# Kernel tuning notes

Measured on AMD Instinct MI355X. Metric: run time of the kernel, lower is better.

Reference implementation:

```python
import jax, jax.numpy as jnp
import numpy as np

N = 20000      # atom nodes
N_LG = 40000   # line-graph nodes (= undirected bonds)
E = 80000      # directed edges in original graph (= 2*N_LG)
E_LG = 200000  # line-graph edges
L = 5          # num_layer
D = 300        # emb_dim
NUM_ATOM, NUM_BOND, NUM_DIR, NUM_CHI = 120, 6, 3, 3
EPS = 1e-5


def setup_inputs() -> dict:
    key = jax.random.key(0)
    ks = jax.random.split(key, 24)
    ri = lambda k, shape, hi: jax.random.randint(k, shape, 0, hi, dtype=jnp.int32)
    nm = lambda k, shape: jax.random.normal(k, shape, dtype=jnp.float32) * 0.02
    inp = {}
    inp["x"] = ri(ks[0], (N, 2), 3)
    inp["edge_index"] = ri(ks[1], (2, E), N)
    inp["edge_attr"] = ri(ks[2], (E, 2), 3)
    inp["lg_x"] = ri(ks[3], (N_LG, 2), 3)
    inp["lg_edge_index"] = ri(ks[4], (2, E_LG), N_LG)
    inp["lg_edge_index_map"] = ri(ks[5], (2, N_LG), N)
    inp["lg_edge_index_map2"] = ri(ks[6], (E_LG,), N)
    # GNN-level embeddings
    inp["node_emb1"] = nm(ks[7], (NUM_ATOM, D))
    inp["node_emb2"] = nm(ks[8], (NUM_CHI, D))
    inp["gnn_edge_emb1"] = nm(ks[9], (NUM_BOND, D))
    inp["gnn_edge_emb2"] = nm(ks[10], (NUM_DIR, D))
    # per-layer main-graph GINConv params (stacked over layers)
    inp["g_emb1"] = nm(ks[11], (L, NUM_BOND, D))
    inp["g_emb2"] = nm(ks[12], (L, NUM_DIR, D))
    inp["g_w1"] = nm(ks[13], (L, D, 2 * D))
    inp["g_b1"] = jnp.zeros((L, 2 * D), jnp.float32)
    inp["g_w2"] = nm(ks[14], (L, 2 * D, D))
    inp["g_b2"] = jnp.zeros((L, D), jnp.float32)
    inp["g_gamma"] = jnp.ones((L, D), jnp.float32)
    inp["g_beta"] = jnp.zeros((L, D), jnp.float32)
    # per-layer line-graph GINConv params (is_lg=True -> atom/chirality tables)
    inp["lg_emb1"] = nm(ks[15], (L, NUM_ATOM, D))
    inp["lg_emb2"] = nm(ks[16], (L, NUM_CHI, D))
    inp["lg_w1"] = nm(ks[17], (L, D, 2 * D))
    inp["lg_b1"] = jnp.zeros((L, 2 * D), jnp.float32)
    inp["lg_w2"] = nm(ks[18], (L, 2 * D, D))
    inp["lg_b2"] = jnp.zeros((L, D), jnp.float32)
    inp["lg_gamma"] = jnp.ones((L, D), jnp.float32)
    inp["lg_beta"] = jnp.zeros((L, D), jnp.float32)
    return inp


def gin_conv(xn, src, dst, ea, emb1, emb2, sl_idx, w1, b1, w2, b2):
    # self loops appended at the end, with self_loop_attr = emb1[sl_idx] + emb2[0]
    n = xn.shape[0]
    sl = jnp.broadcast_to(emb1[sl_idx] + emb2[0], (n, xn.shape[1]))
    ea_full = jnp.concatenate([ea, sl], axis=0)
    idx = jnp.arange(n, dtype=src.dtype)
    src_f = jnp.concatenate([src, idx])
    dst_f = jnp.concatenate([dst, idx])
    msg = xn[src_f] + ea_full                      # gather + add
    aggr = jax.ops.segment_sum(msg, dst_f, num_segments=n)  # scatter-add
    return jnp.maximum(aggr @ w1 + b1, 0.0) @ w2 + b2        # MLP update


def batchnorm(h, g, b):
    # training-mode BN: batch mean / biased variance (matches torch normalization)
    mu = h.mean(0)
    var = h.var(0)
    return (h - mu) * jax.lax.rsqrt(var + EPS) * g + b


def reference(x, edge_index, edge_attr, lg_x, lg_edge_index, lg_edge_index_map,
              lg_edge_index_map2, node_emb1, node_emb2, gnn_edge_emb1, gnn_edge_emb2,
              g_emb1, g_emb2, g_w1, g_b1, g_w2, g_b2, g_gamma, g_beta,
              lg_emb1, lg_emb2, lg_w1, lg_b1, lg_w2, lg_b2, lg_gamma, lg_beta):
    h = node_emb1[x[:, 0]] + node_emb2[x[:, 1]]
    e = gnn_edge_emb1[lg_x[:, 0]] + gnn_edge_emb2[lg_x[:, 1]]
    h_list, e_list = [h], [e]
    lg_src, lg_dst = lg_edge_index[0], lg_edge_index[1]
    for layer in range(L):
        if layer == 0:
            ea = g_emb1[0][edge_attr[:, 0]] + g_emb2[0][edge_attr[:, 1]]
            src, dst = edge_index[0], edge_index[1]
        else:
            # edge_index rewritten from line-graph map; edge_attr = cat([e, e])
            ea = jnp.concatenate([e_list[layer], e_list[layer]], axis=0)
            src = jnp.concatenate([lg_edge_index_map[0], lg_edge_index_map[1]])
            dst = jnp.concatenate([lg_edge_index_map[1], lg_edge_index_map[0]])
        h = gin_conv(h_list[layer], src, dst, ea, g_emb1[layer], g_emb2[layer], 4,
                     g_w1[layer], g_b1[layer], g_w2[layer], g_b2[layer])
        h = batchnorm(h, g_gamma[layer], g_beta[layer])
        if layer < L - 1:
            h = jnp.maximum(h, 0.0)
        h_list.append(h)
        if layer == 0:
            xa = x[lg_edge_index_map2]  # int atom features of shared node
            lg_ea = lg_emb1[0][xa[:, 0]] + lg_emb2[0][xa[:, 1]]
        else:
            # lg_edge_attr = h[lg_edge_index_map2] from the PREVIOUS iteration's h
            lg_ea = h_list[layer][lg_edge_index_map2]
        e = gin_conv(e_list[layer], lg_src, lg_dst, lg_ea, lg_emb1[layer], lg_emb2[layer], 119,
                     lg_w1[layer], lg_b1[layer], lg_w2[layer], lg_b2[layer])
        e = batchnorm(e, lg_gamma[layer], lg_beta[layer])
        if layer < L - 1:
            e = jnp.maximum(e, 0.0)
        e_list.append(e)
    # (h_list, e_list) packed as one array: [L+1, N + N_LG, D]
    return jnp.concatenate([jnp.stack(h_list), jnp.stack(e_list)], axis=1)
```

## Files before the change

### kernel.cpp

```cpp
#include <hip/hip_runtime.h>

#define D 300

namespace {

constexpr int kN   = 20000;
constexpr int kNLG = 40000;
constexpr int kE   = 80000;
constexpr int kELG = 200000;
constexpr int kL   = 5;

constexpr int K1P = 320;
constexpr int N1P = 640;
constexpr int K2P = 640;
constexpr int N2P = 384;
constexpr int MP_N   = 20096;
constexpr int MP_ALL = 60160;
constexpr int MAIN_TILES = 157;
constexpr int RH = 320;
constexpr int RQ = 40;

typedef __attribute__((ext_vector_type(8))) _Float16 half8;
typedef __attribute__((ext_vector_type(2))) _Float16 half2v;
typedef __attribute__((ext_vector_type(4))) float f32x4;

__device__ inline short f2h(float f) {
  _Float16 h = (_Float16)f;
  return __builtin_bit_cast(short, h);
}

__device__ inline float h2f(short s) {
  return (float)__builtin_bit_cast(_Float16, s);
}

__device__ inline float2 upk(unsigned u) {
  half2v h = __builtin_bit_cast(half2v, u);
  return make_float2((float)h.x, (float)h.y);
}

__device__ inline unsigned pk(float a, float b) {
  half2v h;
  h.x = (_Float16)a;
  h.y = (_Float16)b;
  return __builtin_bit_cast(unsigned, h);
}

__device__ inline void addrow(float* acc, uint4 r) {
  float2 t0 = upk(r.x), t1 = upk(r.y), t2 = upk(r.z), t3 = upk(r.w);
  acc[0] += t0.x; acc[1] += t0.y; acc[2] += t1.x; acc[3] += t1.y;
  acc[4] += t2.x; acc[5] += t2.y; acc[6] += t3.x; acc[7] += t3.y;
}

__device__ inline uint4 pk4(const float* a) {
  uint4 r;
  r.x = pk(a[0], a[1]); r.y = pk(a[2], a[3]);
  r.z = pk(a[4], a[5]); r.w = pk(a[6], a[7]);
  return r;
}

__device__ inline void gload_lds16(const void* g, void* l) {
  __builtin_amdgcn_global_load_lds(
      (const __attribute__((address_space(1))) void*)g,
      (__attribute__((address_space(3))) void*)l, 16, 0, 0);
}


__global__ void k_init(float* __restrict__ stats, short* __restrict__ ab,
                       int* __restrict__ m0_cur, int* __restrict__ mL_cur,
                       int* __restrict__ lg_cur) {
  int g = blockIdx.x * blockDim.x + threadIdx.x;
  if (g < kL * 1200) stats[g] = 0.f;
  int np1 = (MP_N - kN) * K1P;
  int np2 = (MP_ALL - MP_N - kNLG) * K1P;
  if (g < np1) ab[(size_t)kN * K1P + g] = 0;
  if (g < np2) ab[(size_t)(MP_N + kNLG) * K1P + g] = 0;
  if (g < kN) { m0_cur[g] = 0; mL_cur[g] = 0; }
  if (g < kNLG) lg_cur[g] = 0;
}


__global__ void k_hist_all(const int* __restrict__ edge_index,
                           const int* __restrict__ lg_map,
                           const int* __restrict__ lg_ei,
// ... 112 lines not shown

__device__ void cvt_w1(const float* W, short* Wt, int g) {
  int per = N1P * K1P;
  int l = g / per, rem = g - l * per;
  int n = rem / K1P, k = rem - n * K1P;
  float v = (n < 2 * D && k < D) ? W[(size_t)l * D * 2 * D + (size_t)k * 2 * D + n] : 0.f;
  Wt[g] = f2h(v);
}

__device__ void cvt_w2(const float* W, short* Wt, int g) {
  int per = N2P * K2P;
  int l = g / per, rem = g - l * per;
  int n = rem / K2P, k = rem - n * K2P;
  float v = (n < D && k < 2 * D) ? W[(size_t)l * 2 * D * D + (size_t)k * D + n] : 0.f;
  Wt[g] = f2h(v);
}

__global__ void k_convert_wt_all(const float* __restrict__ g_w1, const float* __restrict__ g_w2,
                                 const float* __restrict__ lg_w1, const float* __restrict__ lg_w2,
                                 short* __restrict__ g_w1t, short* __restrict__ g_w2t,
                                 short* __restrict__ lg_w1t, short* __restrict__ lg_w2t) {
  int g = blockIdx.x * blockDim.x + threadIdx.x;
  const int s1 = kL * N1P * K1P, s2 = kL * N2P * K2P;
  if (g < s1) { cvt_w1(g_w1, g_w1t, g); return; }
  g -= s1;
  if (g < s2) { cvt_w2(g_w2, g_w2t, g); return; }
  g -= s2;
  if (g < s1) { cvt_w1(lg_w1, lg_w1t, g); return; }
  g -= s1;
  if (g < s2) cvt_w2(lg_w2, lg_w2t, g);
}


__global__ void k_gather_all0(
    const uint4* __restrict__ h16, const uint4* __restrict__ e16,
    const int* __restrict__ m_src, const int* __restrict__ eattr,
    const int* __restrict__ x, const int* __restrict__ lg_src,
    const int* __restrict__ map2,
    const uint4* __restrict__ t1m, const uint4* __restrict__ t2m,
    const uint4* __restrict__ t1l, const uint4* __restrict__ t2l,
    const float* __restrict__ slvM, const float* __restrict__ slvL,
    const int* __restrict__ m_offs, const int* __restrict__ m_perm,
    const int* __restrict__ l_offs, const int* __restrict__ l_perm,
    uint4* __restrict__ ab) {
  int node = blockIdx.x * 4 + (threadIdx.x >> 6);
  int lane = threadIdx.x & 63;
  if (node >= kN + kNLG) return;
  bool act = lane < RQ;
  int ll = act ? lane : 0;
  bool isM = node < kN;
  int j = isM ? node : node - kN;
  const uint4* selfrow = isM ? (h16 + (size_t)node * RQ) : (e16 + (size_t)j * RQ);
  const float* sv = (isM ? slvM : slvL) + ll * 8;
  const int* offs = isM ? m_offs : l_offs;
  const int* permp = isM ? m_perm : l_perm;
  const uint4* bA = isM ? h16 : e16;
  const uint4* bT1 = isM ? t1m : t1l;
  const uint4* bT2 = isM ? t2m : t2l;

  float acc[8];
  {
    uint4 s = selfrow[ll];
    float2 t0 = upk(s.x), t1 = upk(s.y), t2 = upk(s.z), t3 = upk(s.w);
    acc[0] = t0.x + sv[0]; acc[1] = t0.y + sv[1];
    acc[2] = t1.x + sv[2]; acc[3] = t1.y + sv[3];
    acc[4] = t2.x + sv[4]; acc[5] = t2.y + sv[5];
    acc[6] = t3.x + sv[6]; acc[7] = t3.y + sv[7];
  }

  int p0 = offs[j], p1 = offs[j + 1];
  for (int pb = p0; pb < p1; pb += 64) {
    int cnt = min(64, p1 - pb);
    int e_ = permp[pb + ((lane < cnt) ? lane : 0)];
    int r1, r2, r3;
    if (isM) {
      r1 = m_src[e_];
      r2 = eattr[2 * e_];
      r3 = eattr[2 * e_ + 1];
    } else {
      r1 = lg_src[e_];
      int a = map2[e_];
      r2 = x[2 * a];
      r3 = x[2 * a + 1];
    }
    int t = 0;
    for (; t + 1 < cnt; t += 2) {
      int a0 = __shfl(r1, t), b0 = __shfl(r2, t), c0 = __shfl(r3, t);
      int a1 = __shfl(r1, t + 1), b1 = __shfl(r2, t + 1), c1 = __shfl(r3, t + 1);
      uint4 x0 = bA[(size_t)a0 * RQ + ll];
      uint4 y0 = bT1[(size_t)b0 * RQ + ll];
      uint4 z0 = bT2[(size_t)c0 * RQ + ll];
      uint4 x1 = bA[(size_t)a1 * RQ + ll];
      uint4 y1 = bT1[(size_t)b1 * RQ + ll];
      uint4 z1 = bT2[(size_t)c1 * RQ + ll];
      addrow(acc, x0); addrow(acc, y0); addrow(acc, z0);
      addrow(acc, x1); addrow(acc, y1); addrow(acc, z1);
    }
    if (t < cnt) {
      int a0 = __shfl(r1, t), b0 = __shfl(r2, t), c0 = __shfl(r3, t);
      uint4 x0 = bA[(size_t)a0 * RQ + ll];
      uint4 y0 = bT1[(size_t)b0 * RQ + ll];
      uint4 z0 = bT2[(size_t)c0 * RQ + ll];
      addrow(acc, x0); addrow(acc, y0); addrow(acc, z0);
    }
  }
  if (act) ab[(size_t)(isM ? node : MP_N + j) * RQ + ll] = pk4(acc);
}

__global__ void k_gather_allL(
    const uint4* __restrict__ h16, const uint4* __restrict__ e16,
    const int* __restrict__ lg_map, const int* __restrict__ lg_src,
    const int* __restrict__ map2,
    const float* __restrict__ slvM, const float* __restrict__ slvL,
    const int* __restrict__ m_offs, const int* __restrict__ m_perm,
    const int* __restrict__ l_offs, const int* __restrict__ l_perm,
    uint4* __restrict__ ab) {
  int node = blockIdx.x * 4 + (threadIdx.x >> 6);
  int lane = threadIdx.x & 63;
  if (node >= kN + kNLG) return;
  bool act = lane < RQ;
  int ll = act ? lane : 0;
  bool isM = node < kN;
  int j = isM ? node : node - kN;
  const uint4* selfrow = isM ? (h16 + (size_t)node * RQ) : (e16 + (size_t)j * RQ);
  const float* sv = (isM ? slvM : slvL) + ll * 8;
  const int* offs = isM ? m_offs : l_offs;
  const int* permp = isM ? m_perm : l_perm;
  const uint4* bA = isM ? h16 : e16;
  const uint4* bB = isM ? e16 : h16;

  float acc[8];
  {
    uint4 s = selfrow[ll];
    float2 t0 = upk(s.x), t1 = upk(s.y), t2 = upk(s.z), t3 = upk(s.w);
    acc[0] = t0.x + sv[0]; acc[1] = t0.y + sv[1];
    acc[2] = t1.x + sv[2]; acc[3] = t1.y + sv[3];
    acc[4] = t2.x + sv[4]; acc[5] = t2.y + sv[5];
    acc[6] = t3.x + sv[6]; acc[7] = t3.y + sv[7];
  }

  int p0 = offs[j], p1 = offs[j + 1];
  for (int pb = p0; pb < p1; pb += 64) {
    int cnt = min(64, p1 - pb);
    int e_ = permp[pb + ((lane < cnt) ? lane : 0)];
    int ra, rb;
    if (isM) {
      ra = lg_map[e_];
      rb = (e_ < kNLG) ? e_ : e_ - kNLG;
    } else {
      ra = lg_src[e_];
      rb = map2[e_];
    }
    int t = 0;
    for (; t + 3 < cnt; t += 4) {
      int a0 = __shfl(ra, t),     b0 = __shfl(rb, t);
      int a1 = __shfl(ra, t + 1), b1 = __shfl(rb, t + 1);
      int a2 = __shfl(ra, t + 2), b2 = __shfl(rb, t + 2);
      int a3 = __shfl(ra, t + 3), b3 = __shfl(rb, t + 3);
      uint4 x0 = bA[(size_t)a0 * RQ + ll];
      uint4 y0 = bB[(size_t)b0 * RQ + ll];
      uint4 x1 = bA[(size_t)a1 * RQ + ll];
      uint4 y1 = bB[(size_t)b1 * RQ + ll];
      uint4 x2 = bA[(size_t)a2 * RQ + ll];
      uint4 y2 = bB[(size_t)b2 * RQ + ll];
      uint4 x3 = bA[(size_t)a3 * RQ + ll];
      uint4 y3 = bB[(size_t)b3 * RQ + ll];
      addrow(acc, x0); addrow(acc, y0);
      addrow(acc, x1); addrow(acc, y1);
      addrow(acc, x2); addrow(acc, y2);
      addrow(acc, x3); addrow(acc, y3);
    }
    for (; t < cnt; ++t) {
      int a0 = __shfl(ra, t), b0 = __shfl(rb, t);
      uint4 x0 = bA[(size_t)a0 * RQ + ll];
      uint4 y0 = bB[(size_t)b0 * RQ + ll];
      addrow(acc, x0); addrow(acc, y0);
    }
  }
  if (act) ab[(size_t)(isM ? node : MP_N + j) * RQ + ll] = pk4(acc);
}


__global__ void k_embed_pair(const int* __restrict__ idx, const float* __restrict__ t1,
                             const float* __restrict__ t2, float* __restrict__ out,
                             short* __restrict__ hist, int n) {
  int g = blockIdx.x * blockDim.x + threadIdx.x;
  if (g >= n * RH) return;
  int i = g / RH, c = g - i * RH;
  short hv = 0;
  if (c < D) {
    float v = t1[(size_t)idx[2 * i] * D + c] + t2[(size_t)idx[2 * i + 1] * D + c];
    out[(size_t)i * D + c] = v;
    hv = f2h(v);
  }
  hist[g] = hv;
}


template<bool RELU, bool STATS>
__global__ __launch_bounds__(256) void k_mfma_gemm_dual(
    const short* __restrict__ A,
    const short* __restrict__ BtM, const short* __restrict__ BtL,
    const float* __restrict__ biasM, const float* __restrict__ biasL, int biasN,
    short* __restrict__ Cout, int Ccols, int Cstride, int Kpad,
    int mainLimit, int lgLimit,
    float* __restrict__ statsM, float* __restrict__ statsL) {
  __shared__ __align__(16) short ldsA[128 * 32];
  __shared__ __align__(16) short ldsB[128 * 32];
  __shared__ float sd[256];
  const int tid = threadIdx.x;
  const int lane = tid & 63, w = tid >> 6;
  const bool isMain = (int)blockIdx.y < MAIN_TILES;
  const short* Bt = isMain ? BtM : BtL;
  const float* bias = isMain ? biasM : biasL;
  const int rowLimit = isMain ? mainLimit : lgLimit;
  const int brow = blockIdx.y * 128;
  const int bcol = blockIdx.x * 128;
  const int wr = w >> 1, wc = w & 1;

  if (STATS) sd[tid] = 0.f;

  f32x4 acc[4][4] = {};

  const int sr = tid >> 2;
  const int sc = (tid & 3) * 8;
  char* la = (char*)ldsA + w * 1024;
  char* lb = (char*)ldsB + w * 1024;

  for (int k0 = 0; k0 < Kpad; k0 += 32) {
    __syncthreads();
    const short* gA0 = A + (size_t)(brow + sr) * Kpad + (k0 + sc);
    const short* gB0 = Bt + (size_t)(bcol + sr) * Kpad + (k0 + sc);
    gload_lds16(gA0, la);
    gload_lds16(gA0 + (size_t)64 * Kpad, la + 4096);
    gload_lds16(gB0, lb);
    gload_lds16(gB0 + (size_t)64 * Kpad, lb + 4096);
    __syncthreads();
// ... 2 lines not shown
    half8 af[4], bf[4];
#pragma unroll
    for (int m = 0; m < 4; ++m) {
      int row = wr * 64 + m * 16 + (lane & 15);
      af[m] = *(const half8*)((const char*)ldsA + row * 64 + kq);
    }
#pragma unroll
    for (int n = 0; n < 4; ++n) {
      int col = wc * 64 + n * 16 + (lane & 15);
      bf[n] = *(const half8*)((const char*)ldsB + col * 64 + kq);
    }
#pragma unroll
    for (int m = 0; m < 4; ++m)
#pragma unroll
      for (int n = 0; n < 4; ++n)
        acc[m][n] = __builtin_amdgcn_mfma_f32_16x16x32_f16(af[m], bf[n], acc[m][n], 0, 0, 0);
  }

  const int r0 = brow + wr * 64;
  const int c0 = bcol + wc * 64;
  float ps[4] = {}, pq[4] = {};
#pragma unroll
  for (int m = 0; m < 4; ++m) {
#pragma unroll
    for (int i = 0; i < 4; ++i) {
      int row = r0 + m * 16 + (lane >> 4) * 4 + i;
      bool rv = row < rowLimit;
#pragma unroll
      for (int n = 0; n < 4; ++n) {
        int col = c0 + n * 16 + (lane & 15);
        float bv = (col < biasN) ? bias[col] : 0.f;
        float v = acc[m][n][i] + bv;
        if (RELU) v = fmaxf(v, 0.f);
        if (rv && col < Ccols) {
          Cout[(size_t)row * Cstride + col] = f2h(v);
          if (STATS) { ps[n] += v; pq[n] += v * v; }
        }
      }
    }
  }

  if (STATS) {
#pragma unroll
    for (int n = 0; n < 4; ++n) {
      float s = ps[n], q = pq[n];
      s += __shfl_xor(s, 16); q += __shfl_xor(q, 16);
      s += __shfl_xor(s, 32); q += __shfl_xor(q, 32);
      if ((lane >> 4) == 0) {
        int c = wc * 64 + n * 16 + (lane & 15);
        atomicAdd(&sd[c], s);
        atomicAdd(&sd[128 + c], q);
      }
    }
    __syncthreads();
    float* gs = isMain ? statsM : statsL;
    if (tid < 128) {
      int col = bcol + tid;
      if (col < Ccols) {
        atomicAdd(&gs[col], sd[tid]);
        atomicAdd(&gs[D + col], sd[128 + tid]);
      }
    }
  }
}


template<bool WRITE_HIST>
__global__ void k_bn_apply_all(const short* __restrict__ pre, float* __restrict__ Xout,
                               short* __restrict__ hist,
                               const float* __restrict__ statsM,
                               const float* __restrict__ statsL,
                               const float* __restrict__ gM, const float* __restrict__ bM,
                               const float* __restrict__ gL, const float* __restrict__ bL,
                               int relu) {
  int g = blockIdx.x * blockDim.x + threadIdx.x;
  if (g >= (kN + kNLG) * RH) return;
  int r = g / RH;
  int c = g - r * RH;
  short hv = 0;
  if (c < D) {
    bool m = r < kN;
    int pr = m ? r : MP_N + (r - kN);
    const float* s = m ? statsM : statsL;
    float inv_n = m ? (1.f / kN) : (1.f / kNLG);
    float mu = s[c] * inv_n;
    float var = s[D + c] * inv_n - mu * mu;
    float rs = rsqrtf(var + 1e-5f);
    float gam = (m ? gM : gL)[c];
    float bet = (m ? bM : bL)[c];
    float v = (h2f(pre[(size_t)pr * N2P + c]) - mu) * rs * gam + bet;
    if (relu) v = fmaxf(v, 0.f);
    Xout[(size_t)r * D + c] = v;
    hv = f2h(v);
  }
  if (WRITE_HIST) hist[g] = hv;
}

}

extern "C" void kernel_launch(void* const* d_in, const int* in_sizes, int n_in,
                              void* d_out_v, int out_size, void* d_ws, size_t ws_size,
                              hipStream_t stream) {
  const int*   x            = (const int*)d_in[0];
  const int*   edge_index   = (const int*)d_in[1];
  const int*   edge_attr    = (const int*)d_in[2];
  const int*   lg_x         = (const int*)d_in[3];
  const int*   lg_edge_index= (const int*)d_in[4];
  const int*   lg_map       = (const int*)d_in[5];
  const int*   lg_map2      = (const int*)d_in[6];
  const float* node_emb1    = (const float*)d_in[7];
  const float* node_emb2    = (const float*)d_in[8];
  const float* gnn_e_emb1   = (const float*)d_in[9];
  const float* gnn_e_emb2   = (const float*)d_in[10];
  const float* g_emb1       = (const float*)d_in[11];
  const float* g_emb2       = (const float*)d_in[12];
  const float* g_w1         = (const float*)d_in[13];
  const float* g_b1         = (const float*)d_in[14];
  const float* g_w2         = (const float*)d_in[15];
  const float* g_b2         = (const float*)d_in[16];
  const float* g_gamma      = (const float*)d_in[17];
  const float* g_beta       = (const float*)d_in[18];
  const float* lg_emb1      = (const float*)d_in[19];
  const float* lg_emb2      = (const float*)d_in[20];
  const float* lg_w1        = (const float*)d_in[21];
  const float* lg_b1        = (const float*)d_in[22];
  const float* lg_w2        = (const float*)d_in[23];
  const float* lg_b2        = (const float*)d_in[24];
  const float* lg_gamma     = (const float*)d_in[25];
  const float* lg_beta      = (const float*)d_in[26];

  float* out = (float*)d_out_v;
  char*  ws  = (char*)d_ws;

  size_t off = 0;
  auto alloc = [&](size_t bytes) { void* p = ws + off; off = (off + bytes + 255) & ~(size_t)255; return p; };
  short* ab      = (short*)alloc((size_t)MP_ALL * K1P * 2);
  short* hidden  = (short*)alloc((size_t)MP_ALL * N1P * 2);
  short* pre16   = (short*)alloc((size_t)MP_ALL * N2P * 2);
  short* hist16  = (short*)alloc((size_t)(kL + 1) * 60000 * RH * 2);
  short* g_w1t   = (short*)alloc((size_t)kL * N1P * K1P * 2);
  short* g_w2t   = (short*)alloc((size_t)kL * N2P * K2P * 2);
  short* lg_w1t  = (short*)alloc((size_t)kL * N1P * K1P * 2);
  short* lg_w2t  = (short*)alloc((size_t)kL * N2P * K2P * 2);
  float* stats   = (float*)alloc(kL * 1200 * 4);
  float* slv     = (float*)alloc(kL * 640 * 4);
  short* t1m     = (short*)alloc(6 * RH * 2);
  short* t2m     = (short*)alloc(3 * RH * 2);
  short* t1l     = (short*)alloc(120 * RH * 2);
  short* t2l     = (short*)alloc(3 * RH * 2);
  int* m0_offs = (int*)alloc((kN + 1) * 4);
  int* m0_cur  = (int*)alloc(kN * 4);
  int* m0_perm = (int*)alloc(kE * 4);
  int* mL_offs = (int*)alloc((kN + 1) * 4);
  int* mL_cur  = (int*)alloc(kN * 4);
  int* mL_perm = (int*)alloc(2 * kNLG * 4);
  int* lg_offs = (int*)alloc((kNLG + 1) * 4);
  int* lg_cur  = (int*)alloc(kNLG * 4);
  int* lg_perm = (int*)alloc(kELG * 4);

  auto hptr  = [&](int l) { return out + (size_t)l * 60000 * D; };
  auto h16p  = [&](int l) { return hist16 + (size_t)l * 60000 * RH; };
  auto e16p  = [&](int l) { return hist16 + ((size_t)l * 60000 + kN) * RH; };

  dim3 b(256);

  k_init<<<(kNLG + 255) / 256, b, 0, stream>>>(stats, ab, m0_cur, mL_cur, lg_cur);
  {
    int tot = kE + 2 * kNLG + kELG;
    k_hist_all<<<(tot + 255) / 256, b, 0, stream>>>(edge_index, lg_map, lg_edge_index,
                                                    m0_cur, mL_cur, lg_cur);
    k_scan3<<<3, b, 0, stream>>>(m0_cur, m0_offs, mL_cur, mL_offs, lg_cur, lg_offs);
    k_fill_all<<<(tot + 255) / 256, b, 0, stream>>>(edge_index, lg_map, lg_edge_index,
                                                    m0_cur, m0_perm, mL_cur, mL_perm,
                                                    lg_cur, lg_perm);
  }
  k_selfvec<<<(kL * 640 + 255) / 256, b, 0, stream>>>(g_emb1, g_emb2, lg_emb1, lg_emb2, slv);
  k_pad_tab_all<<<(132 * RH + 255) / 256, b, 0, stream>>>(g_emb1, g_emb2, lg_emb1, lg_emb2,
                                                          t1m, t2m, t1l, t2l);
  {
    int tot = 2 * kL * (N1P * K1P + N2P * K2P);
    k_convert_wt_all<<<(tot + 255) / 256, b, 0, stream>>>(g_w1, g_w2, lg_w1, lg_w2,
                                                          g_w1t, g_w2t, lg_w1t, lg_w2t);
  }
  k_embed_pair<<<(kN * RH + 255) / 256, b, 0, stream>>>(x, node_emb1, node_emb2,
                                                        hptr(0), h16p(0), kN);
  k_embed_pair<<<(kNLG * RH + 255) / 256, b, 0, stream>>>(lg_x, gnn_e_emb1, gnn_e_emb2,
                                                          hptr(0) + (size_t)kN * D,
                                                          e16p(0), kNLG);

  for (int l = 0; l < kL; ++l) {
    int relu_tail = (l < kL - 1) ? 1 : 0;
    float* slot = stats + (size_t)l * 1200;
    const float* slvM = slv + (size_t)l * 640;
    const float* slvL = slvM + 320;

    if (l == 0)
      k_gather_all0<<<(kN + kNLG + 3) / 4, b, 0, stream>>>(
          (const uint4*)h16p(0), (const uint4*)e16p(0),
          edge_index, edge_attr, x, lg_edge_index, lg_map2,
          (const uint4*)t1m, (const uint4*)t2m, (const uint4*)t1l, (const uint4*)t2l,
          slvM, slvL, m0_offs, m0_perm, lg_offs, lg_perm, (uint4*)ab);
    else
      k_gather_allL<<<(kN + kNLG + 3) / 4, b, 0, stream>>>(
          (const uint4*)h16p(l), (const uint4*)e16p(l),
          lg_map, lg_edge_index, lg_map2,
          slvM, slvL, mL_offs, mL_perm, lg_offs, lg_perm, (uint4*)ab);

    k_mfma_gemm_dual<true, false><<<dim3(N1P / 128, MP_ALL / 128), b, 0, stream>>>(
        ab, g_w1t + (size_t)l * N1P * K1P, lg_w1t + (size_t)l * N1P * K1P,
        g_b1 + (size_t)l * 2 * D, lg_b1 + (size_t)l * 2 * D, 2 * D,
        hidden, N1P, N1P, K1P, MP_ALL, MP_ALL, nullptr, nullptr);

    k_mfma_gemm_dual<false, true><<<dim3(N2P / 128, MP_ALL / 128), b, 0, stream>>>(
        hidden, g_w2t + (size_t)l * N2P * K2P, lg_w2t + (size_t)l * N2P * K2P,
        g_b2 + (size_t)l * D, lg_b2 + (size_t)l * D, D,
        pre16, D, N2P, K2P, kN, MP_N + kNLG,
        slot, slot + 600);

    if (l < kL - 1)
      k_bn_apply_all<true><<<((kN + kNLG) * RH + 255) / 256, b, 0, stream>>>(
          pre16, hptr(l + 1), h16p(l + 1), slot, slot + 600,
          g_gamma + (size_t)l * D, g_beta + (size_t)l * D,
          lg_gamma + (size_t)l * D, lg_beta + (size_t)l * D, relu_tail);
    else
      k_bn_apply_all<false><<<((kN + kNLG) * RH + 255) / 256, b, 0, stream>>>(
          pre16, hptr(l + 1), h16p(l + 1), slot, slot + 600,
          g_gamma + (size_t)l * D, g_beta + (size_t)l * D,
          lg_gamma + (size_t)l * D, lg_beta + (size_t)l * D, relu_tail);
  }
}
```

Measured before the change: 1.539 ms.

## Fuse batchnorm apply into next layer's gather, drop fp16 history buffers

Removes the per-layer batchnorm-apply kernel. The next layer's gather now reads the raw fp16 GEMM output, recomputes the BN scale and shift from the stats, and applies BN plus ReLU to every gathered neighbour row. The self-row pass writes the fp32 output for the previous layer, and a separate final kernel handles the last layer without ReLU. The second GEMM now writes a narrower 320-column pre-activation buffer instead of 384. This saves a full read/write pass and the fp16 history storage per layer. In exchange, the gather does extra FMA and max work per neighbour and the unroll drops from 4 to 2.

```diff
diff --git a/kernel.cpp b/kernel.cpp
--- a/kernel.cpp
+++ b/kernel.cpp
@@ -14,6 +14,7 @@
 constexpr int N1P = 640;
 constexpr int K2P = 640;
 constexpr int N2P = 384;
+constexpr int PQH = 320;
 constexpr int MP_N   = 20096;
 constexpr int MP_ALL = 60160;
 constexpr int MAIN_TILES = 157;
@@ -49,6 +50,12 @@
   float2 t0 = upk(r.x), t1 = upk(r.y), t2 = upk(r.z), t3 = upk(r.w);
   acc[0] += t0.x; acc[1] += t0.y; acc[2] += t1.x; acc[3] += t1.y;
   acc[4] += t2.x; acc[5] += t2.y; acc[6] += t3.x; acc[7] += t3.y;
+}
+
+__device__ inline void unpk8(uint4 r, float* v) {
+  float2 t0 = upk(r.x), t1 = upk(r.y), t2 = upk(r.z), t3 = upk(r.w);
+  v[0] = t0.x; v[1] = t0.y; v[2] = t1.x; v[3] = t1.y;
+  v[4] = t2.x; v[5] = t2.y; v[6] = t3.x; v[7] = t3.y;
 }
 
 __device__ inline uint4 pk4(const float* a) {
@@ -255,12 +262,10 @@
 
   float acc[8];
   {
-    uint4 s = selfrow[ll];
-    float2 t0 = upk(s.x), t1 = upk(s.y), t2 = upk(s.z), t3 = upk(s.w);
-    acc[0] = t0.x + sv[0]; acc[1] = t0.y + sv[1];
-    acc[2] = t1.x + sv[2]; acc[3] = t1.y + sv[3];
-    acc[4] = t2.x + sv[4]; acc[5] = t2.y + sv[5];
-    acc[6] = t3.x + sv[6]; acc[7] = t3.y + sv[7];
+    float vv[8];
+    unpk8(selfrow[ll], vv);
+#pragma unroll
+    for (int i = 0; i < 8; ++i) acc[i] = vv[i] + sv[i];
   }
 
   int p0 = offs[j], p1 = offs[j + 1];
@@ -302,14 +307,18 @@
   if (act) ab[(size_t)(isM ? node : MP_N + j) * RQ + ll] = pk4(acc);
 }
 
-__global__ void k_gather_allL(
-    const uint4* __restrict__ h16, const uint4* __restrict__ e16,
+
+__global__ void k_gather_bn(
+    const uint4* __restrict__ pre,
     const int* __restrict__ lg_map, const int* __restrict__ lg_src,
     const int* __restrict__ map2,
+    const float* __restrict__ sM, const float* __restrict__ sL,
+    const float* __restrict__ gaM, const float* __restrict__ beM,
+    const float* __restrict__ gaL, const float* __restrict__ beL,
     const float* __restrict__ slvM, const float* __restrict__ slvL,
     const int* __restrict__ m_offs, const int* __restrict__ m_perm,
     const int* __restrict__ l_offs, const int* __restrict__ l_perm,
-    uint4* __restrict__ ab) {
+    float* __restrict__ outF, uint4* __restrict__ ab) {
   int node = blockIdx.x * 4 + (threadIdx.x >> 6);
   int lane = threadIdx.x & 63;
   if (node >= kN + kNLG) return;
@@ -317,59 +326,97 @@
   int ll = act ? lane : 0;
   bool isM = node < kN;
   int j = isM ? node : node - kN;
-  const uint4* selfrow = isM ? (h16 + (size_t)node * RQ) : (e16 + (size_t)j * RQ);
+
+  float aM[8], bM[8], aL[8], bL[8];
+#pragma unroll
+  for (int i = 0; i < 8; ++i) {
+    int c = ll * 8 + i;
+    if (c < D) {
+      float muM = sM[c] * (1.f / kN);
+      float vaM = sM[D + c] * (1.f / kN) - muM * muM;
+      float am = rsqrtf(vaM + 1e-5f) * gaM[c];
+      aM[i] = am; bM[i] = beM[c] - muM * am;
+      float muL = sL[c] * (1.f / kNLG);
+      float vaL = sL[D + c] * (1.f / kNLG) - muL * muL;
+      float al = rsqrtf(vaL + 1e-5f) * gaL[c];
+      aL[i] = al; bL[i] = beL[c] - muL * al;
+    } else {
+      aM[i] = bM[i] = aL[i] = bL[i] = 0.f;
+    }
+  }
+
   const float* sv = (isM ? slvM : slvL) + ll * 8;
   const int* offs = isM ? m_offs : l_offs;
   const int* permp = isM ? m_perm : l_perm;
-  const uint4* bA = isM ? h16 : e16;
-  const uint4* bB = isM ? e16 : h16;
 
   float acc[8];
   {
-    uint4 s = selfrow[ll];
-    float2 t0 = upk(s.x), t1 = upk(s.y), t2 = upk(s.z), t3 = upk(s.w);
-    acc[0] = t0.x + sv[0]; acc[1] = t0.y + sv[1];
-    acc[2] = t1.x + sv[2]; acc[3] = t1.y + sv[3];
-    acc[4] = t2.x + sv[4]; acc[5] = t2.y + sv[5];
-    acc[6] = t3.x + sv[6]; acc[7] = t3.y + sv[7];
+    int selfRow = isM ? node : MP_N + j;
+    float vv[8], y[8];
+    unpk8(pre[(size_t)selfRow * RQ + ll], vv);
+#pragma unroll
+    for (int i = 0; i < 8; ++i) {
+      float a = isM ? aM[i] : aL[i];
+      float b = isM ? bM[i] : bL[i];
+      y[i] = fmaxf(a * vv[i] + b, 0.f);
+      acc[i] = y[i] + sv[i];
+    }
+    if (act) {
+      float* op = outF + (size_t)node * D + ll * 8;
+      if (ll < 37) {
+        *(float4*)op = make_float4(y[0], y[1], y[2], y[3]);
+        *(float4*)(op + 4) = make_float4(y[4], y[5], y[6], y[7]);
+      } else if (ll == 37) {
+        *(float4*)op = make_float4(y[0], y[1], y[2], y[3]);
+      }
+    }
   }
 
   int p0 = offs[j], p1 = offs[j + 1];
   for (int pb = p0; pb < p1; pb += 64) {
     int cnt = min(64, p1 - pb);
     int e_ = permp[pb + ((lane < cnt) ? lane : 0)];
-    int ra, rb;
+    int rh, re;
     if (isM) {
-      ra = lg_map[e_];
-      rb = (e_ < kNLG) ? e_ : e_ - kNLG;
+      rh = lg_map[e_];
+      re = MP_N + ((e_ < kNLG) ? e_ : e_ - kNLG);
     } else {
-      ra = lg_src[e_];
-      rb = map2[e_];
+      rh = map2[e_];
+      re = MP_N + lg_src[e_];
     }
     int t = 0;
-    for (; t + 3 < cnt; t += 4) {
-      int a0 = __shfl(ra, t),     b0 = __shfl(rb, t);
-      int a1 = __shfl(ra, t + 1), b1 = __shfl(rb, t + 1);
-      int a2 = __shfl(ra, t + 2), b2 = __shfl(rb, t + 2);
-      int a3 = __shfl(ra, t + 3), b3 = __shfl(rb, t + 3);
-      uint4 x0 = bA[(size_t)a0 * RQ + ll];
-      uint4 y0 = bB[(size_t)b0 * RQ + ll];
-      uint4 x1 = bA[(size_t)a1 * RQ + ll];
-      uint4 y1 = bB[(size_t)b1 * RQ + ll];
-      uint4 x2 = bA[(size_t)a2 * RQ + ll];
-      uint4 y2 = bB[(size_t)b2 * RQ + ll];
-      uint4 x3 = bA[(size_t)a3 * RQ + ll];
-      uint4 y3 = bB[(size_t)b3 * RQ + ll];
-      addrow(acc, x0); addrow(acc, y0);
-      addrow(acc, x1); addrow(acc, y1);
-      addrow(acc, x2); addrow(acc, y2);
-      addrow(acc, x3); addrow(acc, y3);
-    }
-    for (; t < cnt; ++t) {
-      int a0 = __shfl(ra, t), b0 = __shfl(rb, t);
-      uint4 x0 = bA[(size_t)a0 * RQ + ll];
-      uint4 y0 = bB[(size_t)b0 * RQ + ll];
-      addrow(acc, x0); addrow(acc, y0);
+    for (; t + 1 < cnt; t += 2) {
+      int h0 = __shfl(rh, t),     e0 = __shfl(re, t);
+      int h1 = __shfl(rh, t + 1), e1 = __shfl(re, t + 1);
+      uint4 xh0 = pre[(size_t)h0 * RQ + ll];
+      uint4 xe0 = pre[(size_t)e0 * RQ + ll];
+      uint4 xh1 = pre[(size_t)h1 * RQ + ll];
+      uint4 xe1 = pre[(size_t)e1 * RQ + ll];
+      float v[8];
+      unpk8(xh0, v);
+#pragma unroll
+      for (int i = 0; i < 8; ++i) acc[i] += fmaxf(aM[i] * v[i] + bM[i], 0.f);
+      unpk8(xe0, v);
+#pragma unroll
+      for (int i = 0; i < 8; ++i) acc[i] += fmaxf(aL[i] * v[i] + bL[i], 0.f);
+      unpk8(xh1, v);
+#pragma unroll
+      for (int i = 0; i < 8; ++i) acc[i] += fmaxf(aM[i] * v[i] + bM[i], 0.f);
+      unpk8(xe1, v);
+#pragma unroll
+      for (int i = 0; i < 8; ++i) acc[i] += fmaxf(aL[i] * v[i] + bL[i], 0.f);
+    }
+    if (t < cnt) {
+      int h0 = __shfl(rh, t), e0 = __shfl(re, t);
+      uint4 xh0 = pre[(size_t)h0 * RQ + ll];
+      uint4 xe0 = pre[(size_t)e0 * RQ + ll];
+      float v[8];
+      unpk8(xh0, v);
+#pragma unroll
+      for (int i = 0; i < 8; ++i) acc[i] += fmaxf(aM[i] * v[i] + bM[i], 0.f);
+      unpk8(xe0, v);
+#pragma unroll
+      for (int i = 0; i < 8; ++i) acc[i] += fmaxf(aL[i] * v[i] + bL[i], 0.f);
     }
   }
   if (act) ab[(size_t)(isM ? node : MP_N + j) * RQ + ll] = pk4(acc);
@@ -397,7 +444,7 @@
     const short* __restrict__ A,
     const short* __restrict__ BtM, const short* __restrict__ BtL,
     const float* __restrict__ biasM, const float* __restrict__ biasL, int biasN,
-    short* __restrict__ Cout, int Ccols, int Cstride, int Kpad,
+    short* __restrict__ Cout, int Cstat, int Cwrite, int Cstride, int Kpad,
     int mainLimit, int lgLimit,
     float* __restrict__ statsM, float* __restrict__ statsL) {
   __shared__ __align__(16) short ldsA[128 * 32];
@@ -466,9 +513,9 @@
         float bv = (col < biasN) ? bias[col] : 0.f;
         float v = acc[m][n][i] + bv;
         if (RELU) v = fmaxf(v, 0.f);
-        if (rv && col < Ccols) {
+        if (rv && col < Cwrite) {
           Cout[(size_t)row * Cstride + col] = f2h(v);
-          if (STATS) { ps[n] += v; pq[n] += v * v; }
+          if (STATS && col < Cstat) { ps[n] += v; pq[n] += v * v; }
         }
       }
     }
@@ -490,7 +537,7 @@
     float* gs = isMain ? statsM : statsL;
     if (tid < 128) {
       int col = bcol + tid;
-      if (col < Ccols) {
+      if (col < Cstat) {
         atomicAdd(&gs[col], sd[tid]);
         atomicAdd(&gs[D + col], sd[128 + tid]);
       }
@@ -499,35 +546,24 @@
 }
 
 
-template<bool WRITE_HIST>
-__global__ void k_bn_apply_all(const short* __restrict__ pre, float* __restrict__ Xout,
-                               short* __restrict__ hist,
-                               const float* __restrict__ statsM,
-                               const float* __restrict__ statsL,
-                               const float* __restrict__ gM, const float* __restrict__ bM,
-                               const float* __restrict__ gL, const float* __restrict__ bL,
-                               int relu) {
+__global__ void k_bn_final(const short* __restrict__ pre, float* __restrict__ Xout,
+                           const float* __restrict__ sM, const float* __restrict__ sL,
+                           const float* __restrict__ gM, const float* __restrict__ bM,
+                           const float* __restrict__ gL, const float* __restrict__ bL) {
   int g = blockIdx.x * blockDim.x + threadIdx.x;
-  if (g >= (kN + kNLG) * RH) return;
-  int r = g / RH;
-  int c = g - r * RH;
-  short hv = 0;
-  if (c < D) {
-    bool m = r < kN;
-    int pr = m ? r : MP_N + (r - kN);
-    const float* s = m ? statsM : statsL;
-    float inv_n = m ? (1.f / kN) : (1.f / kNLG);
-    float mu = s[c] * inv_n;
-    float var = s[D + c] * inv_n - mu * mu;
-    float rs = rsqrtf(var + 1e-5f);
-    float gam = (m ? gM : gL)[c];
-    float bet = (m ? bM : bL)[c];
-    float v = (h2f(pre[(size_t)pr * N2P + c]) - mu) * rs * gam + bet;
-    if (relu) v = fmaxf(v, 0.f);
-    Xout[(size_t)r * D + c] = v;
-    hv = f2h(v);
-  }
-  if (WRITE_HIST) hist[g] = hv;
+  if (g >= (kN + kNLG) * D) return;
+  int r = g / D;
+  int c = g - r * D;
+  bool m = r < kN;
+  int pr = m ? r : MP_N + (r - kN);
+  const float* s = m ? sM : sL;
+  float inv_n = m ? (1.f / kN) : (1.f / kNLG);
+  float mu = s[c] * inv_n;
+  float var = s[D + c] * inv_n - mu * mu;
+  float rs = rsqrtf(var + 1e-5f);
+  float gam = (m ? gM : gL)[c];
+  float bet = (m ? bM : bL)[c];
+  Xout[g] = (h2f(pre[(size_t)pr * PQH + c]) - mu) * rs * gam + bet;
 }
 
 }
@@ -570,8 +606,8 @@
   auto alloc = [&](size_t bytes) { void* p = ws + off; off = (off + bytes + 255) & ~(size_t)255; return p; };
   short* ab      = (short*)alloc((size_t)MP_ALL * K1P * 2);
   short* hidden  = (short*)alloc((size_t)MP_ALL * N1P * 2);
-  short* pre16   = (short*)alloc((size_t)MP_ALL * N2P * 2);
-  short* hist16  = (short*)alloc((size_t)(kL + 1) * 60000 * RH * 2);
+  short* pre16   = (short*)alloc((size_t)MP_ALL * PQH * 2);
+  short* init16  = (short*)alloc((size_t)60000 * RH * 2);
   short* g_w1t   = (short*)alloc((size_t)kL * N1P * K1P * 2);
   short* g_w2t   = (short*)alloc((size_t)kL * N2P * K2P * 2);
   short* lg_w1t  = (short*)alloc((size_t)kL * N1P * K1P * 2);
@@ -592,9 +628,7 @@
   int* lg_cur  = (int*)alloc(kNLG * 4);
   int* lg_perm = (int*)alloc(kELG * 4);
 
-  auto hptr  = [&](int l) { return out + (size_t)l * 60000 * D; };
-  auto h16p  = [&](int l) { return hist16 + (size_t)l * 60000 * RH; };
-  auto e16p  = [&](int l) { return hist16 + ((size_t)l * 60000 + kN) * RH; };
+  auto hptr = [&](int l) { return out + (size_t)l * 60000 * D; };
 
   dim3 b(256);
 
@@ -617,49 +651,50 @@
                                                           g_w1t, g_w2t, lg_w1t, lg_w2t);
   }
   k_embed_pair<<<(kN * RH + 255) / 256, b, 0, stream>>>(x, node_emb1, node_emb2,
-                                                        hptr(0), h16p(0), kN);
+                                                        hptr(0), init16, kN);
   k_embed_pair<<<(kNLG * RH + 255) / 256, b, 0, stream>>>(lg_x, gnn_e_emb1, gnn_e_emb2,
                                                           hptr(0) + (size_t)kN * D,
-                                                          e16p(0), kNLG);
+                                                          init16 + (size_t)kN * RH, kNLG);
 
   for (int l = 0; l < kL; ++l) {
-    int relu_tail = (l < kL - 1) ? 1 : 0;
     float* slot = stats + (size_t)l * 1200;
     const float* slvM = slv + (size_t)l * 640;
     const float* slvL = slvM + 320;
 
-    if (l == 0)
+    if (l == 0) {
       k_gather_all0<<<(kN + kNLG + 3) / 4, b, 0, stream>>>(
-          (const uint4*)h16p(0), (const uint4*)e16p(0),
+          (const uint4*)init16, (const uint4*)(init16 + (size_t)kN * RH),
           edge_index, edge_attr, x, lg_edge_index, lg_map2,
           (const uint4*)t1m, (const uint4*)t2m, (const uint4*)t1l, (const uint4*)t2l,
           slvM, slvL, m0_offs, m0_perm, lg_offs, lg_perm, (uint4*)ab);
-    else
-      k_gather_allL<<<(kN + kNLG + 3) / 4, b, 0, stream>>>(
-          (const uint4*)h16p(l), (const uint4*)e16p(l),
-          lg_map, lg_edge_index, lg_map2,
-          slvM, slvL, mL_offs, mL_perm, lg_offs, lg_perm, (uint4*)ab);
+    } else {
+      float* pslot = stats + (size_t)(l - 1) * 1200;
+      k_gather_bn<<<(kN + kNLG + 3) / 4, b, 0, stream>>>(
+          (const uint4*)pre16, lg_map, lg_edge_index, lg_map2,
+          pslot, pslot + 600,
+          g_gamma + (size_t)(l - 1) * D, g_beta + (size_t)(l - 1) * D,
+          lg_gamma + (size_t)(l - 1) * D, lg_beta + (size_t)(l - 1) * D,
+          slvM, slvL, mL_offs, mL_perm, lg_offs, lg_perm,
+          hptr(l), (uint4*)ab);
+    }
 
     k_mfma_gemm_dual<true, false><<<dim3(N1P / 128, MP_ALL / 128), b, 0, stream>>>(
         ab, g_w1t + (size_t)l * N1P * K1P, lg_w1t + (size_t)l * N1P * K1P,
         g_b1 + (size_t)l * 2 * D, lg_b1 + (size_t)l * 2 * D, 2 * D,
-        hidden, N1P, N1P, K1P, MP_ALL, MP_ALL, nullptr, nullptr);
+        hidden, 0, N1P, N1P, K1P, MP_ALL, MP_ALL, nullptr, nullptr);
 
     k_mfma_gemm_dual<false, true><<<dim3(N2P / 128, MP_ALL / 128), b, 0, stream>>>(
         hidden, g_w2t + (size_t)l * N2P * K2P, lg_w2t + (size_t)l * N2P * K2P,
         g_b2 + (size_t)l * D, lg_b2 + (size_t)l * D, D,
-        pre16, D, N2P, K2P, kN, MP_N + kNLG,
+        pre16, D, PQH, PQH, K2P, kN, MP_N + kNLG,
         slot, slot + 600);
-
-    if (l < kL - 1)
-      k_bn_apply_all<true><<<((kN + kNLG) * RH + 255) / 256, b, 0, stream>>>(
-          pre16, hptr(l + 1), h16p(l + 1), slot, slot + 600,
-          g_gamma + (size_t)l * D, g_beta + (size_t)l * D,
-          lg_gamma + (size_t)l * D, lg_beta + (size_t)l * D, relu_tail);
-    else
-      k_bn_apply_all<false><<<((kN + kNLG) * RH + 255) / 256, b, 0, stream>>>(
-          pre16, hptr(l + 1), h16p(l + 1), slot, slot + 600,
-          g_gamma + (size_t)l * D, g_beta + (size_t)l * D,
-          lg_gamma + (size_t)l * D, lg_beta + (size_t)l * D, relu_tail);
-  }
-}
+  }
+
+  {
+    float* slot = stats + (size_t)(kL - 1) * 1200;
+    k_bn_final<<<((kN + kNLG) * D + 255) / 256, b, 0, stream>>>(
+        pre16, hptr(kL), slot, slot + 600,
+        g_gamma + (size_t)(kL - 1) * D, g_beta + (size_t)(kL - 1) * D,
+        lg_gamma + (size_t)(kL - 1) * D, lg_beta + (size_t)(kL - 1) * D);
+  }
+}
```

Result: slower. 2.276 ms (+47.9%).

## Vectorize batchnorm apply and embedding, precompute BN coefficients, double-buffer fp16 history

Applied to the files above, without the earlier changes.

Replaces the per-element batchnorm apply kernel with a vectorized one that handles 8 halves per thread, using per-column scale and shift computed once by a new small k_bn_coef kernel. The pre-activation buffer stride shrinks from 384 to 320 halves. The two embedding launches are merged into one vectorized kernel, and the fp16 history moves from a per-layer array to two ping-pong slots. The aim is fewer, wider memory transactions, no repeated mean/var/rsqrt per element, and a smaller workspace, at the cost of one extra tiny launch per layer.

```diff
diff --git a/kernel.cpp b/kernel.cpp
--- a/kernel.cpp
+++ b/kernel.cpp
@@ -14,11 +14,13 @@
 constexpr int N1P = 640;
 constexpr int K2P = 640;
 constexpr int N2P = 384;
+constexpr int PQH = 320;
 constexpr int MP_N   = 20096;
 constexpr int MP_ALL = 60160;
 constexpr int MAIN_TILES = 157;
 constexpr int RH = 320;
 constexpr int RQ = 40;
+constexpr int NALL = kN + kNLG;
 
 typedef __attribute__((ext_vector_type(8))) _Float16 half8;
 typedef __attribute__((ext_vector_type(2))) _Float16 half2v;
@@ -27,10 +29,6 @@
 __device__ inline short f2h(float f) {
   _Float16 h = (_Float16)f;
   return __builtin_bit_cast(short, h);
-}
-
-__device__ inline float h2f(short s) {
-  return (float)__builtin_bit_cast(_Float16, s);
 }
 
 __device__ inline float2 upk(unsigned u) {
@@ -49,6 +47,12 @@
   float2 t0 = upk(r.x), t1 = upk(r.y), t2 = upk(r.z), t3 = upk(r.w);
   acc[0] += t0.x; acc[1] += t0.y; acc[2] += t1.x; acc[3] += t1.y;
   acc[4] += t2.x; acc[5] += t2.y; acc[6] += t3.x; acc[7] += t3.y;
+}
+
+__device__ inline void unpk8(uint4 r, float* v) {
+  float2 t0 = upk(r.x), t1 = upk(r.y), t2 = upk(r.z), t3 = upk(r.w);
+  v[0] = t0.x; v[1] = t0.y; v[2] = t1.x; v[3] = t1.y;
+  v[4] = t2.x; v[5] = t2.y; v[6] = t3.x; v[7] = t3.y;
 }
 
 __device__ inline uint4 pk4(const float* a) {
@@ -227,6 +231,36 @@
 }
 
 
+__global__ void k_embed_all(const int* __restrict__ x, const int* __restrict__ lg_x,
+                            const float* __restrict__ t1m, const float* __restrict__ t2m,
+                            const float* __restrict__ t1l, const float* __restrict__ t2l,
+                            float* __restrict__ outF, uint4* __restrict__ hist) {
+  int g = blockIdx.x * blockDim.x + threadIdx.x;
+  if (g >= NALL * RQ) return;
+  int r = g / RQ, q = g - r * RQ;
+  bool m = r < kN;
+  int i = m ? r : r - kN;
+  const int* ix = (m ? x : lg_x) + 2 * i;
+  const float* t1 = (m ? t1m : t1l) + (size_t)ix[0] * D;
+  const float* t2 = (m ? t2m : t2l) + (size_t)ix[1] * D;
+  int c0 = q * 8;
+  float y[8] = {0.f, 0.f, 0.f, 0.f, 0.f, 0.f, 0.f, 0.f};
+  if (c0 < D) {
+    float4 p0 = *(const float4*)(t1 + c0);
+    float4 q0 = *(const float4*)(t2 + c0);
+    y[0] = p0.x + q0.x; y[1] = p0.y + q0.y; y[2] = p0.z + q0.z; y[3] = p0.w + q0.w;
+    *(float4*)(outF + (size_t)r * D + c0) = make_float4(y[0], y[1], y[2], y[3]);
+    if (c0 + 8 <= D) {
+      float4 p1 = *(const float4*)(t1 + c0 + 4);
+      float4 q1 = *(const float4*)(t2 + c0 + 4);
+      y[4] = p1.x + q1.x; y[5] = p1.y + q1.y; y[6] = p1.z + q1.z; y[7] = p1.w + q1.w;
+      *(float4*)(outF + (size_t)r * D + c0 + 4) = make_float4(y[4], y[5], y[6], y[7]);
+    }
+  }
+  hist[(size_t)r * RQ + q] = pk4(y);
+}
+
+
 __global__ void k_gather_all0(
     const uint4* __restrict__ h16, const uint4* __restrict__ e16,
     const int* __restrict__ m_src, const int* __restrict__ eattr,
@@ -240,7 +274,7 @@
     uint4* __restrict__ ab) {
   int node = blockIdx.x * 4 + (threadIdx.x >> 6);
   int lane = threadIdx.x & 63;
-  if (node >= kN + kNLG) return;
+  if (node >= NALL) return;
   bool act = lane < RQ;
   int ll = act ? lane : 0;
   bool isM = node < kN;
@@ -255,12 +289,10 @@
 
   float acc[8];
   {
-    uint4 s = selfrow[ll];
-    float2 t0 = upk(s.x), t1 = upk(s.y), t2 = upk(s.z), t3 = upk(s.w);
-    acc[0] = t0.x + sv[0]; acc[1] = t0.y + sv[1];
-    acc[2] = t1.x + sv[2]; acc[3] = t1.y + sv[3];
-    acc[4] = t2.x + sv[4]; acc[5] = t2.y + sv[5];
-    acc[6] = t3.x + sv[6]; acc[7] = t3.y + sv[7];
+    float vv[8];
+    unpk8(selfrow[ll], vv);
+#pragma unroll
+    for (int i = 0; i < 8; ++i) acc[i] = vv[i] + sv[i];
   }
 
   int p0 = offs[j], p1 = offs[j + 1];
@@ -302,6 +334,7 @@
   if (act) ab[(size_t)(isM ? node : MP_N + j) * RQ + ll] = pk4(acc);
 }
 
+
 __global__ void k_gather_allL(
     const uint4* __restrict__ h16, const uint4* __restrict__ e16,
     const int* __restrict__ lg_map, const int* __restrict__ lg_src,
@@ -312,7 +345,7 @@
     uint4* __restrict__ ab) {
   int node = blockIdx.x * 4 + (threadIdx.x >> 6);
   int lane = threadIdx.x & 63;
-  if (node >= kN + kNLG) return;
+  if (node >= NALL) return;
   bool act = lane < RQ;
   int ll = act ? lane : 0;
   bool isM = node < kN;
@@ -326,12 +359,10 @@
 
   float acc[8];
   {
-    uint4 s = selfrow[ll];
-    float2 t0 = upk(s.x), t1 = upk(s.y), t2 = upk(s.z), t3 = upk(s.w);
-    acc[0] = t0.x + sv[0]; acc[1] = t0.y + sv[1];
-    acc[2] = t1.x + sv[2]; acc[3] = t1.y + sv[3];
-    acc[4] = t2.x + sv[4]; acc[5] = t2.y + sv[5];
-    acc[6] = t3.x + sv[6]; acc[7] = t3.y + sv[7];
+    float vv[8];
+    unpk8(selfrow[ll], vv);
+#pragma unroll
+    for (int i = 0; i < 8; ++i) acc[i] = vv[i] + sv[i];
   }
 
   int p0 = offs[j], p1 = offs[j + 1];
@@ -376,28 +407,12 @@
 }
 
 
-__global__ void k_embed_pair(const int* __restrict__ idx, const float* __restrict__ t1,
-                             const float* __restrict__ t2, float* __restrict__ out,
-                             short* __restrict__ hist, int n) {
-  int g = blockIdx.x * blockDim.x + threadIdx.x;
-  if (g >= n * RH) return;
-  int i = g / RH, c = g - i * RH;
-  short hv = 0;
-  if (c < D) {
-    float v = t1[(size_t)idx[2 * i] * D + c] + t2[(size_t)idx[2 * i + 1] * D + c];
-    out[(size_t)i * D + c] = v;
-    hv = f2h(v);
-  }
-  hist[g] = hv;
-}
-
-
 template<bool RELU, bool STATS>
 __global__ __launch_bounds__(256) void k_mfma_gemm_dual(
     const short* __restrict__ A,
     const short* __restrict__ BtM, const short* __restrict__ BtL,
     const float* __restrict__ biasM, const float* __restrict__ biasL, int biasN,
-    short* __restrict__ Cout, int Ccols, int Cstride, int Kpad,
+    short* __restrict__ Cout, int Cstat, int Cwrite, int Cstride, int Kpad,
     int mainLimit, int lgLimit,
     float* __restrict__ statsM, float* __restrict__ statsL) {
   __shared__ __align__(16) short ldsA[128 * 32];
@@ -466,9 +481,9 @@
         float bv = (col < biasN) ? bias[col] : 0.f;
         float v = acc[m][n][i] + bv;
         if (RELU) v = fmaxf(v, 0.f);
-        if (rv && col < Ccols) {
+        if (rv && col < Cwrite) {
           Cout[(size_t)row * Cstride + col] = f2h(v);
-          if (STATS) { ps[n] += v; pq[n] += v * v; }
+          if (STATS && col < Cstat) { ps[n] += v; pq[n] += v * v; }
         }
       }
     }
@@ -490,7 +505,7 @@
     float* gs = isMain ? statsM : statsL;
     if (tid < 128) {
       int col = bcol + tid;
-      if (col < Ccols) {
+      if (col < Cstat) {
         atomicAdd(&gs[col], sd[tid]);
         atomicAdd(&gs[D + col], sd[128 + tid]);
       }
@@ -499,35 +514,60 @@
 }
 
 
-template<bool WRITE_HIST>
-__global__ void k_bn_apply_all(const short* __restrict__ pre, float* __restrict__ Xout,
-                               short* __restrict__ hist,
-                               const float* __restrict__ statsM,
-                               const float* __restrict__ statsL,
-                               const float* __restrict__ gM, const float* __restrict__ bM,
-                               const float* __restrict__ gL, const float* __restrict__ bL,
-                               int relu) {
-  int g = blockIdx.x * blockDim.x + threadIdx.x;
-  if (g >= (kN + kNLG) * RH) return;
-  int r = g / RH;
-  int c = g - r * RH;
-  short hv = 0;
+__global__ void k_bn_coef(const float* __restrict__ stats,
+                          const float* __restrict__ gM, const float* __restrict__ bM,
+                          const float* __restrict__ gL, const float* __restrict__ bL,
+                          float* __restrict__ coef) {
+  int t = blockIdx.x * blockDim.x + threadIdx.x;
+  if (t >= 640) return;
+  bool m = t < 320;
+  int c = m ? t : t - 320;
+  float a = 0.f, b = 0.f;
   if (c < D) {
-    bool m = r < kN;
-    int pr = m ? r : MP_N + (r - kN);
-    const float* s = m ? statsM : statsL;
+    const float* s = stats + (m ? 0 : 600);
     float inv_n = m ? (1.f / kN) : (1.f / kNLG);
     float mu = s[c] * inv_n;
     float var = s[D + c] * inv_n - mu * mu;
-    float rs = rsqrtf(var + 1e-5f);
-    float gam = (m ? gM : gL)[c];
-    float bet = (m ? bM : bL)[c];
-    float v = (h2f(pre[(size_t)pr * N2P + c]) - mu) * rs * gam + bet;
-    if (relu) v = fmaxf(v, 0.f);
-    Xout[(size_t)r * D + c] = v;
-    hv = f2h(v);
-  }
-  if (WRITE_HIST) hist[g] = hv;
+    a = rsqrtf(var + 1e-5f) * (m ? gM : gL)[c];
+    b = (m ? bM : bL)[c] - mu * a;
+  }
+  int base = m ? 0 : 640;
+  coef[base + c] = a;
+  coef[base + 320 + c] = b;
+}
+
+
+template<bool RELU, bool WRITE_HIST>
+__global__ void k_bn_apply_v(const uint4* __restrict__ pre, const float* __restrict__ coef,
+                             float* __restrict__ outF, uint4* __restrict__ hist) {
+  int g = blockIdx.x * blockDim.x + threadIdx.x;
+  if (g >= NALL * RQ) return;
+  int r = g / RQ, q = g - r * RQ;
+  bool m = r < kN;
+  int pr = m ? r : MP_N + (r - kN);
+  float v[8], y[8];
+  unpk8(pre[(size_t)pr * RQ + q], v);
+  const float* cb = coef + (m ? 0 : 640);
+  float4 a0 = *(const float4*)(cb + q * 8);
+  float4 a1 = *(const float4*)(cb + q * 8 + 4);
+  float4 b0 = *(const float4*)(cb + 320 + q * 8);
+  float4 b1 = *(const float4*)(cb + 320 + q * 8 + 4);
+  y[0] = a0.x * v[0] + b0.x; y[1] = a0.y * v[1] + b0.y;
+  y[2] = a0.z * v[2] + b0.z; y[3] = a0.w * v[3] + b0.w;
+  y[4] = a1.x * v[4] + b1.x; y[5] = a1.y * v[5] + b1.y;
+  y[6] = a1.z * v[6] + b1.z; y[7] = a1.w * v[7] + b1.w;
+  if (RELU) {
+#pragma unroll
+    for (int i = 0; i < 8; ++i) y[i] = fmaxf(y[i], 0.f);
+  }
+  float* op = outF + (size_t)r * D + q * 8;
+  if (q < 37) {
+    *(float4*)op = make_float4(y[0], y[1], y[2], y[3]);
+    *(float4*)(op + 4) = make_float4(y[4], y[5], y[6], y[7]);
+  } else if (q == 37) {
+    *(float4*)op = make_float4(y[0], y[1], y[2], y[3]);
+  }
+  if (WRITE_HIST) hist[(size_t)r * RQ + q] = pk4(y);
 }
 
 }
@@ -570,14 +610,15 @@
   auto alloc = [&](size_t bytes) { void* p = ws + off; off = (off + bytes + 255) & ~(size_t)255; return p; };
   short* ab      = (short*)alloc((size_t)MP_ALL * K1P * 2);
   short* hidden  = (short*)alloc((size_t)MP_ALL * N1P * 2);
-  short* pre16   = (short*)alloc((size_t)MP_ALL * N2P * 2);
-  short* hist16  = (short*)alloc((size_t)(kL + 1) * 60000 * RH * 2);
+  short* pre16   = (short*)alloc((size_t)MP_ALL * PQH * 2);
+  short* hist2   = (short*)alloc((size_t)2 * NALL * RH * 2);
   short* g_w1t   = (short*)alloc((size_t)kL * N1P * K1P * 2);
   short* g_w2t   = (short*)alloc((size_t)kL * N2P * K2P * 2);
   short* lg_w1t  = (short*)alloc((size_t)kL * N1P * K1P * 2);
   short* lg_w2t  = (short*)alloc((size_t)kL * N2P * K2P * 2);
   float* stats   = (float*)alloc(kL * 1200 * 4);
   float* slv     = (float*)alloc(kL * 640 * 4);
+  float* coef    = (float*)alloc(1280 * 4);
   short* t1m     = (short*)alloc(6 * RH * 2);
   short* t2m     = (short*)alloc(3 * RH * 2);
   short* t1l     = (short*)alloc(120 * RH * 2);
@@ -592,9 +633,9 @@
   int* lg_cur  = (int*)alloc(kNLG * 4);
   int* lg_perm = (int*)alloc(kELG * 4);
 
-  auto hptr  = [&](int l) { return out + (size_t)l * 60000 * D; };
-  auto h16p  = [&](int l) { return hist16 + (size_t)l * 60000 * RH; };
-  auto e16p  = [&](int l) { return hist16 + ((size_t)l * 60000 + kN) * RH; };
+  auto hptr = [&](int l) { return out + (size_t)l * 60000 * D; };
+  auto slot_h = [&](int s) { return hist2 + (size_t)s * NALL * RH; };
+  auto slot_e = [&](int s) { return hist2 + (size_t)s * NALL * RH + (size_t)kN * RH; };
 
   dim3 b(256);
 
@@ -616,50 +657,50 @@
     k_convert_wt_all<<<(tot + 255) / 256, b, 0, stream>>>(g_w1, g_w2, lg_w1, lg_w2,
                                                           g_w1t, g_w2t, lg_w1t, lg_w2t);
   }
-  k_embed_pair<<<(kN * RH + 255) / 256, b, 0, stream>>>(x, node_emb1, node_emb2,
-                                                        hptr(0), h16p(0), kN);
-  k_embed_pair<<<(kNLG * RH + 255) / 256, b, 0, stream>>>(lg_x, gnn_e_emb1, gnn_e_emb2,
-                                                          hptr(0) + (size_t)kN * D,
-                                                          e16p(0), kNLG);
-
+  k_embed_all<<<(NALL * RQ + 255) / 256, b, 0, stream>>>(x, lg_x, node_emb1, node_emb2,
+                                                         gnn_e_emb1, gnn_e_emb2,
+                                                         hptr(0), (uint4*)slot_h(0));
+
+  int cur = 0;
   for (int l = 0; l < kL; ++l) {
-    int relu_tail = (l < kL - 1) ? 1 : 0;
     float* slot = stats + (size_t)l * 1200;
     const float* slvM = slv + (size_t)l * 640;
     const float* slvL = slvM + 320;
 
     if (l == 0)
-      k_gather_all0<<<(kN + kNLG + 3) / 4, b, 0, stream>>>(
-          (const uint4*)h16p(0), (const uint4*)e16p(0),
+      k_gather_all0<<<(NALL + 3) / 4, b, 0, stream>>>(
+          (const uint4*)slot_h(cur), (const uint4*)slot_e(cur),
           edge_index, edge_attr, x, lg_edge_index, lg_map2,
           (const uint4*)t1m, (const uint4*)t2m, (const uint4*)t1l, (const uint4*)t2l,
           slvM, slvL, m0_offs, m0_perm, lg_offs, lg_perm, (uint4*)ab);
     else
-      k_gather_allL<<<(kN + kNLG + 3) / 4, b, 0, stream>>>(
-          (const uint4*)h16p(l), (const uint4*)e16p(l),
+      k_gather_allL<<<(NALL + 3) / 4, b, 0, stream>>>(
+          (const uint4*)slot_h(cur), (const uint4*)slot_e(cur),
           lg_map, lg_edge_index, lg_map2,
           slvM, slvL, mL_offs, mL_perm, lg_offs, lg_perm, (uint4*)ab);
 
     k_mfma_gemm_dual<true, false><<<dim3(N1P / 128, MP_ALL / 128), b, 0, stream>>>(
         ab, g_w1t + (size_t)l * N1P * K1P, lg_w1t + (size_t)l * N1P * K1P,
         g_b1 + (size_t)l * 2 * D, lg_b1 + (size_t)l * 2 * D, 2 * D,
-        hidden, N1P, N1P, K1P, MP_ALL, MP_ALL, nullptr, nullptr);
+        hidden, 0, N1P, N1P, K1P, MP_ALL, MP_ALL, nullptr, nullptr);
 
     k_mfma_gemm_dual<false, true><<<dim3(N2P / 128, MP_ALL / 128), b, 0, stream>>>(
         hidden, g_w2t + (size_t)l * N2P * K2P, lg_w2t + (size_t)l * N2P * K2P,
         g_b2 + (size_t)l * D, lg_b2 + (size_t)l * D, D,
-        pre16, D, N2P, K2P, kN, MP_N + kNLG,
+        pre16, D, PQH, PQH, K2P, kN, MP_N + kNLG,
         slot, slot + 600);
 
+    k_bn_coef<<<3, b, 0, stream>>>(slot,
+                                   g_gamma + (size_t)l * D, g_beta + (size_t)l * D,
+                                   lg_gamma + (size_t)l * D, lg_beta + (size_t)l * D, coef);
+
+    int nxt = cur ^ 1;
     if (l < kL - 1)
-      k_bn_apply_all<true><<<((kN + kNLG) * RH + 255) / 256, b, 0, stream>>>(
-          pre16, hptr(l + 1), h16p(l + 1), slot, slot + 600,
-          g_gamma + (size_t)l * D, g_beta + (size_t)l * D,
-          lg_gamma + (size_t)l * D, lg_beta + (size_t)l * D, relu_tail);
+      k_bn_apply_v<true, true><<<(NALL * RQ + 255) / 256, b, 0, stream>>>(
+          (const uint4*)pre16, coef, hptr(l + 1), (uint4*)slot_h(nxt));
     else
-      k_bn_apply_all<false><<<((kN + kNLG) * RH + 255) / 256, b, 0, stream>>>(
-          pre16, hptr(l + 1), h16p(l + 1), slot, slot + 600,
-          g_gamma + (size_t)l * D, g_beta + (size_t)l * D,
-          lg_gamma + (size_t)l * D, lg_beta + (size_t)l * D, relu_tail);
-  }
-}
+      k_bn_apply_v<false, false><<<(NALL * RQ + 255) / 256, b, 0, stream>>>(
+          (const uint4*)pre16, coef, hptr(l + 1), (uint4*)slot_h(nxt));
+    cur = nxt;
+  }
+}
```

After: 1.458 ms. 5.2% less time.
